# Kernel tuning notes

Measured on AMD Instinct MI355X. Metric: run time of the kernel, lower is better.

Reference implementation:

```python
import jax, jax.numpy as jnp
import numpy as np

D_MODEL = 1024
NUM_HEADS = 16
DEPTH = D_MODEL // NUM_HEADS
B, S = 2, 2048


def setup_inputs() -> dict:
    key = jax.random.key(0)
    k1, k2, k3 = jax.random.split(key, 3)
    x = jax.random.normal(k1, (B, S, D_MODEL), dtype=jnp.float32)
    # causal mask: 1.0 where attention is disallowed (upper triangle)
    causal = 1.0 - jnp.tril(jnp.ones((S, S), dtype=jnp.float32))
    mask = causal[None, None, :, :]  # [1,1,S,S]
    w_attn = jax.random.normal(k2, (D_MODEL, 3 * D_MODEL), dtype=jnp.float32) * 0.02
    b_attn = jnp.zeros((3 * D_MODEL,), dtype=jnp.float32)
    w_proj = jax.random.normal(k3, (D_MODEL, D_MODEL), dtype=jnp.float32) * 0.02
    b_proj = jnp.zeros((D_MODEL,), dtype=jnp.float32)
    return {"x": x, "mask": mask, "w_attn": w_attn, "b_attn": b_attn,
            "w_proj": w_proj, "b_proj": b_proj}


def _split_heads(t):
    # [B,S,D] -> [B,H,S,depth]
    b, s, _ = t.shape
    return t.reshape(b, s, NUM_HEADS, DEPTH).transpose(0, 2, 1, 3)


def reference(x, mask, w_attn, b_attn, w_proj, b_proj):
    # QKV projection (Conv1d == pointwise dense over last axis)
    qkv = jnp.einsum('bsd,de->bse', x, w_attn) + b_attn
    q, k, v = jnp.split(qkv, 3, axis=2)
    q, k, v = _split_heads(q), _split_heads(k), _split_heads(v)  # [B,H,S,depth]
    present = jnp.stack([k, v], axis=1)  # [B,2,H,S,depth]
    # scaled dot-product attention (inference: no dropout)
    scores = jnp.einsum('bhqd,bhkd->bhqk', q, k) / jnp.sqrt(
        jnp.asarray(DEPTH, dtype=x.dtype))
    scores = scores + mask * (-1e9)
    attn = jax.nn.softmax(scores, axis=-1)
    out = jnp.einsum('bhqk,bhkd->bhqd', attn, v)
    # merge heads: [B,H,S,depth] -> [B,S,D]
    out = out.transpose(0, 2, 1, 3).reshape(x.shape[0], -1, D_MODEL)
    out = jnp.einsum('bsd,de->bse', out, w_proj) + b_proj
    return out, present
```

## Files before the change

### kernel.cpp

```cpp
#include <hip/hip_runtime.h>
#include <stdint.h>

typedef unsigned short u16;
typedef unsigned int u32;
typedef short bf16x8 __attribute__((ext_vector_type(8)));
typedef float f32x4 __attribute__((ext_vector_type(4)));
typedef float f32x16 __attribute__((ext_vector_type(16)));

#define SEQ 2048
#define NH 16
#define DM 1024
#define DEPTH 64

#define QSCALE 0.18033688f
#define SMAX 16.0f

__device__ __forceinline__ u16 f2bf(float f) {
  union { float f; u32 i; } v; v.f = f;
  u32 x = v.i;
  x += 0x7fffu + ((x >> 16) & 1u);
  return (u16)(x >> 16);
}

__device__ __forceinline__ float fexp2(float x) {
#if __has_builtin(__builtin_amdgcn_exp2f)
  return __builtin_amdgcn_exp2f(x);
#else
  return exp2f(x);
#endif
}

__device__ __forceinline__ u32 cvtpk(float lo, float hi) {
  u32 r;
  asm("v_cvt_pk_bf16_f32 %0, %1, %2" : "=v"(r) : "v"(lo), "v"(hi));
  return r;
}
__device__ __forceinline__ float bflo(u32 w) {
  union { u32 i; float f; } u; u.i = w << 16; return u.f;
}
__device__ __forceinline__ float bfhi(u32 w) {
  union { u32 i; float f; } u; u.i = w & 0xffff0000u; return u.f;
}

__device__ __forceinline__ void gload_lds16(const u16* g, u16* l) {
  __builtin_amdgcn_global_load_lds(
      (const __attribute__((address_space(1))) u32*)g,
      (__attribute__((address_space(3))) u32*)l, 16, 0, 0);
}

__global__ __launch_bounds__(256)
void cvt_fused(const float* __restrict__ x, u16* __restrict__ xb,
               const float* __restrict__ wa, const float* __restrict__ wp,
               u16* __restrict__ dwa, u16* __restrict__ dwp) {
  __shared__ float t[32][33];
  const int tid = threadIdx.x;
  int bx = blockIdx.x;
  if (bx < 4096) {
    int i = (bx * 256 + tid) * 4;
    float4 v = *(const float4*)(x + i);
    ushort4 o; o.x = f2bf(v.x); o.y = f2bf(v.y); o.z = f2bf(v.z); o.w = f2bf(v.w);
    *(ushort4*)(xb + i) = o;
    return;
  }
  bx -= 4096;
  const int cx = bx & 127, cy = bx >> 7;
  const float* src; u16* dst; int N, n0;
  if (cx < 96) { src = wa; dst = dwa; N = 3 * DM; n0 = cx << 5; }
  else         { src = wp; dst = dwp; N = DM;     n0 = (cx - 96) << 5; }
  const int k0 = cy << 5;
  const int K = DM;
  {
    int r = tid >> 3, c4 = (tid & 7) << 2;
    float4 v = *(const float4*)(src + (size_t)(k0 + r) * N + n0 + c4);
    t[r][c4 + 0] = v.x; t[r][c4 + 1] = v.y; t[r][c4 + 2] = v.z; t[r][c4 + 3] = v.w;
  }
  __syncthreads();
  {
    int n = tid >> 3, k4 = (tid & 7) << 2;
    ushort4 o;
    o.x = f2bf(t[k4 + 0][n]); o.y = f2bf(t[k4 + 1][n]);
    o.z = f2bf(t[k4 + 2][n]); o.w = f2bf(t[k4 + 3][n]);
    *(ushort4*)(dst + (size_t)(n0 + n) * K + k0 + k4) = o;
  }
}

__global__ __launch_bounds__(256)
void v_transpose(const float* __restrict__ present, u16* __restrict__ vt) {
  __shared__ float t[64][65];
  const int tid = threadIdx.x;
  const int st = blockIdx.x, bh = blockIdx.y;
  const int b = bh >> 4, h = bh & 15;
  const int s0 = st << 6;
  const float* vsrc = present + (((size_t)((b * 2 + 1) * NH + h)) * SEQ + s0) * DEPTH;
  u16* vdst = vt + ((size_t)(b * NH + h) * DEPTH) * SEQ + s0;
#pragma unroll
  for (int i = 0; i < 4; ++i) {
    int e = tid + (i << 8);
    int r = e >> 4, c = e & 15;
    float4 v = *(const float4*)(vsrc + (size_t)r * DEPTH + (c << 2));
    t[r][(c << 2) + 0] = v.x; t[r][(c << 2) + 1] = v.y;
    t[r][(c << 2) + 2] = v.z; t[r][(c << 2) + 3] = v.w;
  }
  __syncthreads();
#pragma unroll
  for (int i = 0; i < 2; ++i) {
    int e = tid + (i << 8);
    int d = e >> 3, s8 = (e & 7) << 3;
    ushort4 o0, o1;
    o0.x = f2bf(t[s8 + 0][d]); o0.y = f2bf(t[s8 + 1][d]);
    o0.z = f2bf(t[s8 + 2][d]); o0.w = f2bf(t[s8 + 3][d]);
    o1.x = f2bf(t[s8 + 4][d]); o1.y = f2bf(t[s8 + 5][d]);
    o1.z = f2bf(t[s8 + 6][d]); o1.w = f2bf(t[s8 + 7][d]);
    *(ushort4*)(vdst + (size_t)d * SEQ + s8) = o0;
    *(ushort4*)(vdst + (size_t)d * SEQ + s8 + 4) = o1;
  }
}

__global__ __launch_bounds__(256)
void gemm_mfma(const u16* __restrict__ A, const u16* __restrict__ Bt,
               const float* __restrict__ bias, int M, int N, int K, int mode,
               float* __restrict__ outf, u16* __restrict__ qws,
               float* __restrict__ present, u16* __restrict__ kbp,
               u16* __restrict__ vtp)
{
  __shared__ __align__(16) u16 As[2][64][64];
  __shared__ __align__(16) u16 Bs[2][128][64];
  const int tid = threadIdx.x;

  const u32 nwg = gridDim.x * gridDim.y;
  const u32 bid0 = blockIdx.y * gridDim.x + blockIdx.x;
  const u32 cpx = nwg >> 3;
  const u32 bid = (bid0 & 7) * cpx + (bid0 >> 3);
  const int m0 = (int)(bid / gridDim.x) << 6;
  const int n0 = (int)(bid % gridDim.x) << 7;

  const int w = tid >> 6, lane = tid & 63;
  const int lane15 = lane & 15, quad = lane >> 4;
  const int wm = (w >> 1) << 5, wn = (w & 1) << 6;

  const int srow = lane >> 3;
  const int sseg = (lane & 7) ^ srow;
  const u16* agbase = A  + (size_t)(m0 + w * 16 + srow) * K + sseg * 8;
  const u16* bgbase = Bt + (size_t)(n0 + w * 32 + srow) * K + sseg * 8;

  const int l7 = lane15 & 7;

  f32x4 acc[2][4] = {};

  const int nk = K >> 6;
#pragma unroll
  for (int i = 0; i < 2; ++i)
    gload_lds16(agbase + (size_t)(i * 8) * K, &As[0][w * 16 + i * 8][0]);
#pragma unroll
  for (int i = 0; i < 4; ++i)
    gload_lds16(bgbase + (size_t)(i * 8) * K, &Bs[0][w * 32 + i * 8][0]);
  __syncthreads();

#pragma unroll 1
  for (int kt = 0; kt < nk; ++kt) {
    const int cur = kt & 1;
    if (kt + 1 < nk) {
      const int kn = (kt + 1) << 6;
#pragma unroll
      for (int i = 0; i < 2; ++i)
        gload_lds16(agbase + (size_t)(i * 8) * K + kn, &As[cur ^ 1][w * 16 + i * 8][0]);
#pragma unroll
      for (int i = 0; i < 4; ++i)
        gload_lds16(bgbase + (size_t)(i * 8) * K + kn, &Bs[cur ^ 1][w * 32 + i * 8][0]);
      asm volatile("s_waitcnt vmcnt(6)" ::: "memory");
    } else {
      asm volatile("s_waitcnt vmcnt(0)" ::: "memory");
    }
    __builtin_amdgcn_sched_barrier(0);
    __builtin_amdgcn_s_barrier();
    __builtin_amdgcn_sched_barrier(0);
#pragma unroll
    for (int ks = 0; ks < 2; ++ks) {
      const int fs = ((ks * 4 + quad) ^ l7) << 3;
      bf16x8 af[2], bfr[4];
#pragma unroll
      for (int tm = 0; tm < 2; ++tm)
        af[tm] = *(const bf16x8*)&As[cur][wm + tm * 16 + lane15][fs];
#pragma unroll
      for (int tn = 0; tn < 4; ++tn)
        bfr[tn] = *(const bf16x8*)&Bs[cur][wn + tn * 16 + lane15][fs];
      __builtin_amdgcn_s_setprio(1);
#pragma unroll
      for (int tm = 0; tm < 2; ++tm)
#pragma unroll
        for (int tn = 0; tn < 4; ++tn)
          acc[tm][tn] = __builtin_amdgcn_mfma_f32_16x16x32_bf16(af[tm], bfr[tn], acc[tm][tn], 0, 0, 0);
      __builtin_amdgcn_s_setprio(0);
    }
    __builtin_amdgcn_sched_barrier(0);
    __builtin_amdgcn_s_barrier();
  }

#pragma unroll
  for (int tn = 0; tn < 4; ++tn) {
    const int c = n0 + wn + tn * 16 + lane15;
    const float bc = bias[c];
    const int t = c >> 10, cc = c & 1023;
    const int h = cc >> 6, d = cc & 63;
#pragma unroll
    for (int tm = 0; tm < 2; ++tm) {
#pragma unroll
      for (int r = 0; r < 4; ++r) {
        const int m = m0 + wm + tm * 16 + quad * 4 + r;
        const float val = acc[tm][tn][r] + bc;
        if (mode == 1) {
          outf[(size_t)m * N + c] = val;
        } else {
          const int b = m >> 11, s = m & 2047;
          if (t == 0) {
            qws[(((size_t)(b * NH + h) * SEQ) + s) * DEPTH + d] = f2bf(val * QSCALE);
          } else {
            const size_t pidx = (((size_t)((b * 2 + (t - 1)) * NH + h) * SEQ) + s) * DEPTH + d;
            present[pidx] = val;
            if (t == 1)
              kbp[(((size_t)(b * NH + h) * SEQ) + s) * DEPTH + d] = f2bf(val);
            else if (vtp)
              vtp[((size_t)(b * NH + h) * DEPTH + d) * SEQ + s] = f2bf(val);
          }
        }
      }
    }
  }
}

__global__ __launch_bounds__(256, 4)
void attn_mfma(const u16* __restrict__ qb, const u16* __restrict__ kb,
               const u16* __restrict__ vt, u16* __restrict__ attnb)
{
  __shared__ __align__(16) u16 Ks[2][64][64];
  __shared__ __align__(16) u16 Vs[2][64][64];

  const int tid = threadIdx.x;
  const int w = tid >> 6, lane = tid & 63;
  const int l31 = lane & 31, hi = lane >> 5;
  const int qh = w >> 1, kh = w & 1;
  const int bh = blockIdx.y;
  const int tt = (blockIdx.x + blockIdx.y) & 31;
  const int b = bh >> 4, h = bh & 15;

  const u16* qbh = qb + ((size_t)(b * NH + h) * SEQ) * DEPTH;
  const u16* kbh = kb + ((size_t)(b * NH + h) * SEQ) * DEPTH;
  const u16* vbh = vt + ((size_t)(b * NH + h) * DEPTH) * SEQ;

  const int srr = lane >> 3;
  const int sseg = (lane & 7) ^ srr;
  const int r0 = w * 16 + srr;
  const int r1 = r0 + 8;
  const int kr0 = (r0 & ~12) | ((r0 & 4) << 1) | ((r0 & 8) >> 1);
  const int kr1 = (r1 & ~12) | ((r1 & 4) << 1) | ((r1 & 8) >> 1);

  const int rbase = kh * 32 + l31;
  const int swz = l31 & 7;

  const int sloc = (tt << 6) + qh * 32 + l31;
  const int nch = tt + 1;

  const int koff0 = ((0 + hi) ^ swz) << 4;
  const int koff1 = ((2 + hi) ^ swz) << 4;
  const int koff2 = ((4 + hi) ^ swz) << 4;
  const int koff3 = ((6 + hi) ^ swz) << 4;
  const int voffA = ((kh * 4 + 0 + hi) ^ swz) << 4;
  const int voffB = ((kh * 4 + 2 + hi) ^ swz) << 4;

  const u16* kgp0 = kbh + (size_t)kr0 * DEPTH + sseg * 8;
  const u16* kgp1 = kbh + (size_t)kr1 * DEPTH + sseg * 8;
  const u16* vgp0 = vbh + (size_t)r0 * SEQ + sseg * 8;
  const u16* vgp1 = vbh + (size_t)r1 * SEQ + sseg * 8;

  gload_lds16(kgp0, &Ks[0][w * 16][0]);
  gload_lds16(kgp1, &Ks[0][w * 16 + 8][0]);
  gload_lds16(vgp0, &Vs[0][w * 16][0]);
  gload_lds16(vgp1, &Vs[0][w * 16 + 8][0]);

  const u16* qrow = qbh + (size_t)sloc * DEPTH + hi * 8;
  bf16x8 qf0 = *(const bf16x8*)(qrow);
  bf16x8 qf1 = *(const bf16x8*)(qrow + 16);
  bf16x8 qf2 = *(const bf16x8*)(qrow + 32);
  bf16x8 qf3 = *(const bf16x8*)(qrow + 48);

  f32x16 accO0 = {};
  f32x16 accO1 = {};
  float L = 0.f;

  __syncthreads();

#pragma unroll 1
  for (int ct = 0; ct < nch; ++ct) {
    const int bb = ct & 1;
    if (ct + 1 < nch) {
      kgp0 += 64 * DEPTH; kgp1 += 64 * DEPTH;
      vgp0 += 64; vgp1 += 64;
      gload_lds16(kgp0, &Ks[bb ^ 1][w * 16][0]);
      gload_lds16(kgp1, &Ks[bb ^ 1][w * 16 + 8][0]);
      gload_lds16(vgp0, &Vs[bb ^ 1][w * 16][0]);
      gload_lds16(vgp1, &Vs[bb ^ 1][w * 16 + 8][0]);
      asm volatile("s_waitcnt vmcnt(4)" ::: "memory");
    } else {
      asm volatile("s_waitcnt vmcnt(0)" ::: "memory");
    }
    __builtin_amdgcn_sched_barrier(0);
    __builtin_amdgcn_s_barrier();
    __builtin_amdgcn_sched_barrier(0);
    const bool atdiag = (ct == tt);
    if (!(atdiag && qh == 0 && kh == 1)) {
      const char* kbase = (const char*)&Ks[bb][rbase][0];
      f32x16 sc;
#pragma unroll
      for (int j = 0; j < 16; ++j) sc[j] = -SMAX;
      {
        bf16x8 af0 = *(const bf16x8*)(kbase + koff0);
        sc = __builtin_amdgcn_mfma_f32_32x32x16_bf16(af0, qf0, sc, 0, 0, 0);
        bf16x8 af1 = *(const bf16x8*)(kbase + koff1);
        sc = __builtin_amdgcn_mfma_f32_32x32x16_bf16(af1, qf1, sc, 0, 0, 0);
        bf16x8 af2 = *(const bf16x8*)(kbase + koff2);
        sc = __builtin_amdgcn_mfma_f32_32x32x16_bf16(af2, qf2, sc, 0, 0, 0);
        bf16x8 af3 = *(const bf16x8*)(kbase + koff3);
        sc = __builtin_amdgcn_mfma_f32_32x32x16_bf16(af3, qf3, sc, 0, 0, 0);
      }
      float pe[16];
      if (atdiag && (qh == kh)) {
#pragma unroll
        for (int j = 0; j < 16; ++j) {
          float e = fexp2(sc[j]);
          if ((16 * (j >> 3) + 8 * hi + (j & 7)) > l31) e = 0.f;
          pe[j] = e;
        }
      } else {
#pragma unroll
        for (int j = 0; j < 16; ++j) pe[j] = fexp2(sc[j]);
      }
      const u32 pk0 = cvtpk(pe[0], pe[1]),   pk1 = cvtpk(pe[2], pe[3]);
      const u32 pk2 = cvtpk(pe[4], pe[5]),   pk3 = cvtpk(pe[6], pe[7]);
      const u32 pk4 = cvtpk(pe[8], pe[9]),   pk5 = cvtpk(pe[10], pe[11]);
      const u32 pk6 = cvtpk(pe[12], pe[13]), pk7 = cvtpk(pe[14], pe[15]);
      float l0 = bflo(pk0) + bfhi(pk0);
      float l1 = bflo(pk1) + bfhi(pk1);
      l0 += bflo(pk2) + bfhi(pk2);
      l1 += bflo(pk3) + bfhi(pk3);
      l0 += bflo(pk4) + bfhi(pk4);
      l1 += bflo(pk5) + bfhi(pk5);
      l0 += bflo(pk6) + bfhi(pk6);
      l1 += bflo(pk7) + bfhi(pk7);
      L += l0 + l1;
      union { u32 u[4]; bf16x8 v; } f0, f1;
      f0.u[0] = pk0; f0.u[1] = pk1; f0.u[2] = pk2; f0.u[3] = pk3;
      f1.u[0] = pk4; f1.u[1] = pk5; f1.u[2] = pk6; f1.u[3] = pk7;
      const char* vbase = (const char*)&Vs[bb][l31][0];
      {
        bf16x8 av0 = *(const bf16x8*)(vbase + voffA);
        accO0 = __builtin_amdgcn_mfma_f32_32x32x16_bf16(av0, f0.v, accO0, 0, 0, 0);
        bf16x8 av1 = *(const bf16x8*)(vbase + 4096 + voffA);
        accO1 = __builtin_amdgcn_mfma_f32_32x32x16_bf16(av1, f0.v, accO1, 0, 0, 0);
        bf16x8 av2 = *(const bf16x8*)(vbase + voffB);
        accO0 = __builtin_amdgcn_mfma_f32_32x32x16_bf16(av2, f1.v, accO0, 0, 0, 0);
        bf16x8 av3 = *(const bf16x8*)(vbase + 4096 + voffB);
        accO1 = __builtin_amdgcn_mfma_f32_32x32x16_bf16(av3, f1.v, accO1, 0, 0, 0);
      }
    }
    __builtin_amdgcn_sched_barrier(0);
    __builtin_amdgcn_s_barrier();
  }

  float Lw = L + __shfl_xor(L, 32);
  float* red  = (float*)&Ks[0][0][0];
  float* redL = (float*)&Vs[0][0][0];
  const int base = qh * 2048 + lane * 4;
  if (kh) {
#pragma unroll
    for (int g = 0; g < 4; ++g) {
      float4 v0 = make_float4(accO0[4 * g], accO0[4 * g + 1], accO0[4 * g + 2], accO0[4 * g + 3]);
      *(float4*)&red[base + g * 256] = v0;
      float4 v1 = make_float4(accO1[4 * g], accO1[4 * g + 1], accO1[4 * g + 2], accO1[4 * g + 3]);
      *(float4*)&red[base + 1024 + g * 256] = v1;
    }
    redL[qh * 64 + lane] = Lw;
  }
  __syncthreads();
  if (!kh) {
    const float li = 1.0f / (Lw + redL[qh * 64 + lane]);
    u16* ob = attnb + ((size_t)(b * SEQ + sloc)) * DM + h * DEPTH;
#pragma unroll
    for (int g = 0; g < 4; ++g) {
      float4 p0 = *(const float4*)&red[base + g * 256];
      ushort4 st0;
      st0.x = f2bf((accO0[4 * g + 0] + p0.x) * li);
      st0.y = f2bf((accO0[4 * g + 1] + p0.y) * li);
      st0.z = f2bf((accO0[4 * g + 2] + p0.z) * li);
      st0.w = f2bf((accO0[4 * g + 3] + p0.w) * li);
      *(ushort4*)(ob + 8 * g + 4 * hi) = st0;
      float4 p1 = *(const float4*)&red[base + 1024 + g * 256];
      ushort4 st1;
      st1.x = f2bf((accO1[4 * g + 0] + p1.x) * li);
      st1.y = f2bf((accO1[4 * g + 1] + p1.y) * li);
      st1.z = f2bf((accO1[4 * g + 2] + p1.z) * li);
      st1.w = f2bf((accO1[4 * g + 3] + p1.w) * li);
      *(ushort4*)(ob + 32 + 8 * g + 4 * hi) = st1;
    }
  }
}

extern "C" void kernel_launch(void* const* d_in, const int* in_sizes, int n_in,
                              void* d_out, int out_size, void* d_ws, size_t ws_size,
                              hipStream_t stream) {
  (void)in_sizes; (void)n_in; (void)out_size;
  const float* x      = (const float*)d_in[0];
  const float* w_attn = (const float*)d_in[2];
  const float* b_attn = (const float*)d_in[3];
  const float* w_proj = (const float*)d_in[4];
  const float* b_proj = (const float*)d_in[5];

  float* out     = (float*)d_out;
  float* present = out + (size_t)2 * SEQ * DM;

  u16* qws   = (u16*)d_ws;
  u16* kbp   = qws + (size_t)4194304;
  u16* xb    = kbp + (size_t)4194304;
  u16* wabT  = xb + (size_t)4194304;
  u16* wpbT  = wabT + (size_t)4194304;
  const bool fused = ws_size >= (size_t)21 * 1024 * 1024 * 2 * 2;
  u16* vtp   = fused ? (wpbT + (size_t)1048576) : xb;
  u16* attnb = fused ? xb : wabT;

  cvt_fused<<<8192, 256, 0, stream>>>(x, xb, w_attn, w_proj, wabT, wpbT);

  gemm_mfma<<<dim3(24, 64), 256, 0, stream>>>(xb, wabT, b_attn,
                                              2 * SEQ, 3 * DM, DM, 0,
                                              nullptr, qws, present, kbp,
                                              fused ? vtp : nullptr);
  if (!fused)
    v_transpose<<<dim3(32, 32), 256, 0, stream>>>(present, vtp);
  attn_mfma<<<dim3(32, 32), 256, 0, stream>>>(qws, kbp, vtp, attnb);
  gemm_mfma<<<dim3(8, 64), 256, 0, stream>>>(attnb, wpbT, b_proj,
                                             2 * SEQ, DM, DM, 1,
                                             out, nullptr, nullptr, nullptr, nullptr);
}
```

Measured before the change: 205.9 us.

## Fuse fp32-to-bf16 activation conversion into QKV GEMM A-tile loads

The separate pass that converted x to bf16 is removed. The QKV GEMM now loads fp32 rows of x into registers, packs them to bf16 with cvt_pk, and writes them into swizzled LDS during the k-loop. The weight-transpose kernel is reduced to weights only. The block-to-tile mapping is also changed to a different XCD-chunked layout. This saves one launch and the write and re-read of the bf16 copy of x, at the cost of more global traffic per A tile and register-staged stores to LDS in the GEMM.

```diff
diff --git a/kernel.cpp b/kernel.cpp
--- a/kernel.cpp
+++ b/kernel.cpp
@@ -49,25 +49,15 @@
 }
 
 __global__ __launch_bounds__(256)
-void cvt_fused(const float* __restrict__ x, u16* __restrict__ xb,
-               const float* __restrict__ wa, const float* __restrict__ wp,
+void cvtT_both(const float* __restrict__ wa, const float* __restrict__ wp,
                u16* __restrict__ dwa, u16* __restrict__ dwp) {
   __shared__ float t[32][33];
   const int tid = threadIdx.x;
-  int bx = blockIdx.x;
-  if (bx < 4096) {
-    int i = (bx * 256 + tid) * 4;
-    float4 v = *(const float4*)(x + i);
-    ushort4 o; o.x = f2bf(v.x); o.y = f2bf(v.y); o.z = f2bf(v.z); o.w = f2bf(v.w);
-    *(ushort4*)(xb + i) = o;
-    return;
-  }
-  bx -= 4096;
-  const int cx = bx & 127, cy = bx >> 7;
+  const int bx = blockIdx.x;
   const float* src; u16* dst; int N, n0;
-  if (cx < 96) { src = wa; dst = dwa; N = 3 * DM; n0 = cx << 5; }
-  else         { src = wp; dst = dwp; N = DM;     n0 = (cx - 96) << 5; }
-  const int k0 = cy << 5;
+  if (bx < 96) { src = wa; dst = dwa; N = 3 * DM; n0 = bx << 5; }
+  else         { src = wp; dst = dwp; N = DM;     n0 = (bx - 96) << 5; }
+  const int k0 = blockIdx.y << 5;
   const int K = DM;
   {
     int r = tid >> 3, c4 = (tid & 7) << 2;
@@ -84,40 +74,9 @@
   }
 }
 
+template <int A32>
 __global__ __launch_bounds__(256)
-void v_transpose(const float* __restrict__ present, u16* __restrict__ vt) {
-  __shared__ float t[64][65];
-  const int tid = threadIdx.x;
-  const int st = blockIdx.x, bh = blockIdx.y;
-  const int b = bh >> 4, h = bh & 15;
-  const int s0 = st << 6;
-  const float* vsrc = present + (((size_t)((b * 2 + 1) * NH + h)) * SEQ + s0) * DEPTH;
-  u16* vdst = vt + ((size_t)(b * NH + h) * DEPTH) * SEQ + s0;
-#pragma unroll
-  for (int i = 0; i < 4; ++i) {
-    int e = tid + (i << 8);
-    int r = e >> 4, c = e & 15;
-    float4 v = *(const float4*)(vsrc + (size_t)r * DEPTH + (c << 2));
-    t[r][(c << 2) + 0] = v.x; t[r][(c << 2) + 1] = v.y;
-    t[r][(c << 2) + 2] = v.z; t[r][(c << 2) + 3] = v.w;
-  }
-  __syncthreads();
-#pragma unroll
-  for (int i = 0; i < 2; ++i) {
-    int e = tid + (i << 8);
-    int d = e >> 3, s8 = (e & 7) << 3;
-    ushort4 o0, o1;
-    o0.x = f2bf(t[s8 + 0][d]); o0.y = f2bf(t[s8 + 1][d]);
-    o0.z = f2bf(t[s8 + 2][d]); o0.w = f2bf(t[s8 + 3][d]);
-    o1.x = f2bf(t[s8 + 4][d]); o1.y = f2bf(t[s8 + 5][d]);
-    o1.z = f2bf(t[s8 + 6][d]); o1.w = f2bf(t[s8 + 7][d]);
-    *(ushort4*)(vdst + (size_t)d * SEQ + s8) = o0;
-    *(ushort4*)(vdst + (size_t)d * SEQ + s8 + 4) = o1;
-  }
-}
-
-__global__ __launch_bounds__(256)
-void gemm_mfma(const u16* __restrict__ A, const u16* __restrict__ Bt,
+void gemm_mfma(const void* __restrict__ Av, const u16* __restrict__ Bt,
                const float* __restrict__ bias, int M, int N, int K, int mode,
                float* __restrict__ outf, u16* __restrict__ qws,
                float* __restrict__ present, u16* __restrict__ kbp,
@@ -127,12 +86,16 @@
   __shared__ __align__(16) u16 Bs[2][128][64];
   const int tid = threadIdx.x;
 
-  const u32 nwg = gridDim.x * gridDim.y;
-  const u32 bid0 = blockIdx.y * gridDim.x + blockIdx.x;
-  const u32 cpx = nwg >> 3;
-  const u32 bid = (bid0 & 7) * cpx + (bid0 >> 3);
-  const int m0 = (int)(bid / gridDim.x) << 6;
-  const int n0 = (int)(bid % gridDim.x) << 7;
+  const u32 gx = gridDim.x, gy = gridDim.y;
+  const u32 bid0 = blockIdx.y * gx + blockIdx.x;
+  const u32 W = gx >> 3;
+  const u32 ych = gy >> 3;
+  const u32 s = bid0 >> 3;
+  const u32 xc = s / (ych * W);
+  const u32 rem = s % (ych * W);
+  const u32 yl = rem / W, xi = rem % W;
+  const int m0 = (int)((bid0 & 7) * ych + yl) << 6;
+  const int n0 = (int)(xc * W + xi) << 7;
 
   const int w = tid >> 6, lane = tid & 63;
   const int lane15 = lane & 15, quad = lane >> 4;
@@ -140,20 +103,51 @@
 
   const int srow = lane >> 3;
   const int sseg = (lane & 7) ^ srow;
-  const u16* agbase = A  + (size_t)(m0 + w * 16 + srow) * K + sseg * 8;
   const u16* bgbase = Bt + (size_t)(n0 + w * 32 + srow) * K + sseg * 8;
 
+  const u16* agbase = nullptr;
+  const float* agp = nullptr;
+  u16 *awA = nullptr, *awB = nullptr;
+  if (A32) {
+    const int arow = tid >> 2;
+    const int acolq = (tid & 3) << 4;
+    agp = (const float*)Av + (size_t)(m0 + arow) * K + acolq;
+    const int h = arow & 7;
+    const int sA = ((tid & 3) << 1) ^ h;
+    const int sB = sA ^ 1;
+    awA = &As[0][arow][sA * 8];
+    awB = &As[0][arow][sB * 8];
+  } else {
+    agbase = (const u16*)Av + (size_t)(m0 + w * 16 + srow) * K + sseg * 8;
+  }
+
   const int l7 = lane15 & 7;
-
   f32x4 acc[2][4] = {};
-
   const int nk = K >> 6;
-#pragma unroll
-  for (int i = 0; i < 2; ++i)
-    gload_lds16(agbase + (size_t)(i * 8) * K, &As[0][w * 16 + i * 8][0]);
-#pragma unroll
-  for (int i = 0; i < 4; ++i)
-    gload_lds16(bgbase + (size_t)(i * 8) * K, &Bs[0][w * 32 + i * 8][0]);
+  float4 av0, av1, av2, av3;
+
+  if (A32) {
+    av0 = *(const float4*)(agp + 0);
+    av1 = *(const float4*)(agp + 4);
+    av2 = *(const float4*)(agp + 8);
+    av3 = *(const float4*)(agp + 12);
+#pragma unroll
+    for (int i = 0; i < 4; ++i)
+      gload_lds16(bgbase + (size_t)(i * 8) * K, &Bs[0][w * 32 + i * 8][0]);
+    uint4 q0 = make_uint4(cvtpk(av0.x, av0.y), cvtpk(av0.z, av0.w),
+                          cvtpk(av1.x, av1.y), cvtpk(av1.z, av1.w));
+    uint4 q1 = make_uint4(cvtpk(av2.x, av2.y), cvtpk(av2.z, av2.w),
+                          cvtpk(av3.x, av3.y), cvtpk(av3.z, av3.w));
+    *(uint4*)awA = q0;
+    *(uint4*)awB = q1;
+  } else {
+#pragma unroll
+    for (int i = 0; i < 2; ++i)
+      gload_lds16(agbase + (size_t)(i * 8) * K, &As[0][w * 16 + i * 8][0]);
+#pragma unroll
+    for (int i = 0; i < 4; ++i)
+      gload_lds16(bgbase + (size_t)(i * 8) * K, &Bs[0][w * 32 + i * 8][0]);
+  }
   __syncthreads();
 
 #pragma unroll 1
@@ -161,13 +155,22 @@
     const int cur = kt & 1;
     if (kt + 1 < nk) {
       const int kn = (kt + 1) << 6;
-#pragma unroll
-      for (int i = 0; i < 2; ++i)
-        gload_lds16(agbase + (size_t)(i * 8) * K + kn, &As[cur ^ 1][w * 16 + i * 8][0]);
+      if (A32) {
+        av0 = *(const float4*)(agp + kn + 0);
+        av1 = *(const float4*)(agp + kn + 4);
+        av2 = *(const float4*)(agp + kn + 8);
+        av3 = *(const float4*)(agp + kn + 12);
+      } else {
+#pragma unroll
+        for (int i = 0; i < 2; ++i)
+          gload_lds16(agbase + (size_t)(i * 8) * K + kn, &As[cur ^ 1][w * 16 + i * 8][0]);
+      }
 #pragma unroll
       for (int i = 0; i < 4; ++i)
         gload_lds16(bgbase + (size_t)(i * 8) * K + kn, &Bs[cur ^ 1][w * 32 + i * 8][0]);
-      asm volatile("s_waitcnt vmcnt(6)" ::: "memory");
+      __builtin_amdgcn_sched_barrier(0);
+      if (A32) asm volatile("s_waitcnt vmcnt(8)" ::: "memory");
+      else     asm volatile("s_waitcnt vmcnt(6)" ::: "memory");
     } else {
       asm volatile("s_waitcnt vmcnt(0)" ::: "memory");
     }
@@ -191,6 +194,16 @@
         for (int tn = 0; tn < 4; ++tn)
           acc[tm][tn] = __builtin_amdgcn_mfma_f32_16x16x32_bf16(af[tm], bfr[tn], acc[tm][tn], 0, 0, 0);
       __builtin_amdgcn_s_setprio(0);
+    }
+    if (A32 && (kt + 1 < nk)) {
+      const int bo = (cur ^ 1) * 4096;
+      uint4 q0 = make_uint4(cvtpk(av0.x, av0.y), cvtpk(av0.z, av0.w),
+                            cvtpk(av1.x, av1.y), cvtpk(av1.z, av1.w));
+      uint4 q1 = make_uint4(cvtpk(av2.x, av2.y), cvtpk(av2.z, av2.w),
+                            cvtpk(av3.x, av3.y), cvtpk(av3.z, av3.w));
+      *(uint4*)(awA + bo) = q0;
+      *(uint4*)(awB + bo) = q1;
+      asm volatile("s_waitcnt lgkmcnt(0)" ::: "memory");
     }
     __builtin_amdgcn_sched_barrier(0);
     __builtin_amdgcn_s_barrier();
@@ -211,16 +224,16 @@
         if (mode == 1) {
           outf[(size_t)m * N + c] = val;
         } else {
-          const int b = m >> 11, s = m & 2047;
+          const int b = m >> 11, s2 = m & 2047;
           if (t == 0) {
-            qws[(((size_t)(b * NH + h) * SEQ) + s) * DEPTH + d] = f2bf(val * QSCALE);
+            qws[(((size_t)(b * NH + h) * SEQ) + s2) * DEPTH + d] = f2bf(val * QSCALE);
           } else {
-            const size_t pidx = (((size_t)((b * 2 + (t - 1)) * NH + h) * SEQ) + s) * DEPTH + d;
+            const size_t pidx = (((size_t)((b * 2 + (t - 1)) * NH + h) * SEQ) + s2) * DEPTH + d;
             present[pidx] = val;
             if (t == 1)
-              kbp[(((size_t)(b * NH + h) * SEQ) + s) * DEPTH + d] = f2bf(val);
+              kbp[(((size_t)(b * NH + h) * SEQ) + s2) * DEPTH + d] = f2bf(val);
             else if (vtp)
-              vtp[((size_t)(b * NH + h) * DEPTH + d) * SEQ + s] = f2bf(val);
+              vtp[((size_t)(b * NH + h) * DEPTH + d) * SEQ + s2] = f2bf(val);
           }
         }
       }
@@ -419,23 +432,22 @@
 
   u16* qws   = (u16*)d_ws;
   u16* kbp   = qws + (size_t)4194304;
-  u16* xb    = kbp + (size_t)4194304;
-  u16* wabT  = xb + (size_t)4194304;
+  u16* attnb = kbp + (size_t)4194304;
+  u16* wabT  = attnb + (size_t)4194304;
   u16* wpbT  = wabT + (size_t)4194304;
   const bool fused = ws_size >= (size_t)21 * 1024 * 1024 * 2 * 2;
-  u16* vtp   = fused ? (wpbT + (size_t)1048576) : xb;
-  u16* attnb = fused ? xb : wabT;
-
-  cvt_fused<<<8192, 256, 0, stream>>>(x, xb, w_attn, w_proj, wabT, wpbT);
-
-  gemm_mfma<<<dim3(24, 64), 256, 0, stream>>>(xb, wabT, b_attn,
-                                              2 * SEQ, 3 * DM, DM, 0,
-                                              nullptr, qws, present, kbp,
-                                              fused ? vtp : nullptr);
-  if (!fused)
-    v_transpose<<<dim3(32, 32), 256, 0, stream>>>(present, vtp);
-  attn_mfma<<<dim3(32, 32), 256, 0, stream>>>(qws, kbp, vtp, attnb);
-  gemm_mfma<<<dim3(8, 64), 256, 0, stream>>>(attnb, wpbT, b_proj,
-                                             2 * SEQ, DM, DM, 1,
-                                             out, nullptr, nullptr, nullptr, nullptr);
-}
+  u16* vtp   = fused ? (wpbT + (size_t)1048576) : attnb;
+  (void)vtp;
+
+  cvtT_both<<<dim3(128, 32), 256, 0, stream>>>(w_attn, w_proj, wabT, wpbT);
+
+  gemm_mfma<1><<<dim3(24, 64), 256, 0, stream>>>((const void*)x, wabT, b_attn,
+                                                 2 * SEQ, 3 * DM, DM, 0,
+                                                 nullptr, qws, present, kbp,
+                                                 fused ? (wpbT + (size_t)1048576) : attnb);
+  u16* vt = fused ? (wpbT + (size_t)1048576) : attnb;
+  attn_mfma<<<dim3(32, 32), 256, 0, stream>>>(qws, kbp, vt, attnb);
+  gemm_mfma<0><<<dim3(8, 64), 256, 0, stream>>>((const void*)attnb, wpbT, b_proj,
+                                                2 * SEQ, DM, DM, 1,
+                                                out, nullptr, nullptr, nullptr, nullptr);
+}
```

Result: slower. 214.9 us (+4.4%).

## Always fuse V transpose into QKV GEMM epilogue and remap block swizzle

Applied to the files above, without the earlier changes.

Removes the workspace-size check and the standalone v_transpose kernel. The QKV GEMM epilogue now always writes the transposed bf16 V buffer, which saves one launch and a full re-read of V from present. It also replaces the XCD block remapping with a chunked scheme: each XCD takes a contiguous band of M rows, walked in narrow column groups, to improve L2 reuse. This assumes the workspace is always large enough for the extra vtp buffer, and the epilogue's strided V stores remain uncoalesced.

```diff
diff --git a/kernel.cpp b/kernel.cpp
--- a/kernel.cpp
+++ b/kernel.cpp
@@ -85,38 +85,6 @@
 }
 
 __global__ __launch_bounds__(256)
-void v_transpose(const float* __restrict__ present, u16* __restrict__ vt) {
-  __shared__ float t[64][65];
-  const int tid = threadIdx.x;
-  const int st = blockIdx.x, bh = blockIdx.y;
-  const int b = bh >> 4, h = bh & 15;
-  const int s0 = st << 6;
-  const float* vsrc = present + (((size_t)((b * 2 + 1) * NH + h)) * SEQ + s0) * DEPTH;
-  u16* vdst = vt + ((size_t)(b * NH + h) * DEPTH) * SEQ + s0;
-#pragma unroll
-  for (int i = 0; i < 4; ++i) {
-    int e = tid + (i << 8);
-    int r = e >> 4, c = e & 15;
-    float4 v = *(const float4*)(vsrc + (size_t)r * DEPTH + (c << 2));
-    t[r][(c << 2) + 0] = v.x; t[r][(c << 2) + 1] = v.y;
-    t[r][(c << 2) + 2] = v.z; t[r][(c << 2) + 3] = v.w;
-  }
-  __syncthreads();
-#pragma unroll
-  for (int i = 0; i < 2; ++i) {
-    int e = tid + (i << 8);
-    int d = e >> 3, s8 = (e & 7) << 3;
-    ushort4 o0, o1;
-    o0.x = f2bf(t[s8 + 0][d]); o0.y = f2bf(t[s8 + 1][d]);
-    o0.z = f2bf(t[s8 + 2][d]); o0.w = f2bf(t[s8 + 3][d]);
-    o1.x = f2bf(t[s8 + 4][d]); o1.y = f2bf(t[s8 + 5][d]);
-    o1.z = f2bf(t[s8 + 6][d]); o1.w = f2bf(t[s8 + 7][d]);
-    *(ushort4*)(vdst + (size_t)d * SEQ + s8) = o0;
-    *(ushort4*)(vdst + (size_t)d * SEQ + s8 + 4) = o1;
-  }
-}
-
-__global__ __launch_bounds__(256)
 void gemm_mfma(const u16* __restrict__ A, const u16* __restrict__ Bt,
                const float* __restrict__ bias, int M, int N, int K, int mode,
                float* __restrict__ outf, u16* __restrict__ qws,
@@ -127,12 +95,18 @@
   __shared__ __align__(16) u16 Bs[2][128][64];
   const int tid = threadIdx.x;
 
-  const u32 nwg = gridDim.x * gridDim.y;
-  const u32 bid0 = blockIdx.y * gridDim.x + blockIdx.x;
-  const u32 cpx = nwg >> 3;
-  const u32 bid = (bid0 & 7) * cpx + (bid0 >> 3);
-  const int m0 = (int)(bid / gridDim.x) << 6;
-  const int n0 = (int)(bid % gridDim.x) << 7;
+  const u32 gx = gridDim.x, gy = gridDim.y;
+  const u32 bid0 = blockIdx.y * gx + blockIdx.x;
+  const u32 W = gx >> 3 ? gx >> 3 : 1;
+  const u32 ych = gy >> 3;
+  const u32 s = bid0 >> 3;
+  const u32 nxch = (gx + W - 1) / W;
+  const u32 xc = s / (ych * W);
+  const u32 rem = s % (ych * W);
+  const u32 yl = rem / W, xi = rem % W;
+  (void)nxch;
+  const int m0 = (int)((bid0 & 7) * ych + yl) << 6;
+  const int n0 = (int)(xc * W + xi) << 7;
 
   const int w = tid >> 6, lane = tid & 63;
   const int lane15 = lane & 15, quad = lane >> 4;
@@ -211,16 +185,16 @@
         if (mode == 1) {
           outf[(size_t)m * N + c] = val;
         } else {
-          const int b = m >> 11, s = m & 2047;
+          const int b = m >> 11, s2 = m & 2047;
           if (t == 0) {
-            qws[(((size_t)(b * NH + h) * SEQ) + s) * DEPTH + d] = f2bf(val * QSCALE);
+            qws[(((size_t)(b * NH + h) * SEQ) + s2) * DEPTH + d] = f2bf(val * QSCALE);
           } else {
-            const size_t pidx = (((size_t)((b * 2 + (t - 1)) * NH + h) * SEQ) + s) * DEPTH + d;
+            const size_t pidx = (((size_t)((b * 2 + (t - 1)) * NH + h) * SEQ) + s2) * DEPTH + d;
             present[pidx] = val;
             if (t == 1)
-              kbp[(((size_t)(b * NH + h) * SEQ) + s) * DEPTH + d] = f2bf(val);
+              kbp[(((size_t)(b * NH + h) * SEQ) + s2) * DEPTH + d] = f2bf(val);
             else if (vtp)
-              vtp[((size_t)(b * NH + h) * DEPTH + d) * SEQ + s] = f2bf(val);
+              vtp[((size_t)(b * NH + h) * DEPTH + d) * SEQ + s2] = f2bf(val);
           }
         }
       }
@@ -422,18 +396,14 @@
   u16* xb    = kbp + (size_t)4194304;
   u16* wabT  = xb + (size_t)4194304;
   u16* wpbT  = wabT + (size_t)4194304;
-  const bool fused = ws_size >= (size_t)21 * 1024 * 1024 * 2 * 2;
-  u16* vtp   = fused ? (wpbT + (size_t)1048576) : xb;
-  u16* attnb = fused ? xb : wabT;
+  u16* vtp   = wpbT + (size_t)1048576;
+  u16* attnb = xb;
 
   cvt_fused<<<8192, 256, 0, stream>>>(x, xb, w_attn, w_proj, wabT, wpbT);
 
   gemm_mfma<<<dim3(24, 64), 256, 0, stream>>>(xb, wabT, b_attn,
                                               2 * SEQ, 3 * DM, DM, 0,
-                                              nullptr, qws, present, kbp,
-                                              fused ? vtp : nullptr);
-  if (!fused)
-    v_transpose<<<dim3(32, 32), 256, 0, stream>>>(present, vtp);
+                                              nullptr, qws, present, kbp, vtp);
   attn_mfma<<<dim3(32, 32), 256, 0, stream>>>(qws, kbp, vtp, attnb);
   gemm_mfma<<<dim3(8, 64), 256, 0, stream>>>(attnb, wpbT, b_proj,
                                              2 * SEQ, DM, DM, 1,
```

Result: no change. 206.3 us (+0.2%).
